# Performance work log

Measured on AMD Instinct MI355X. Metric: run time of the kernel, lower is better.

The kernel has to match this reference:

```python
import jax, jax.numpy as jnp
import numpy as np

ALPHA = 1.702  # ORT swiglu activation constant


def setup_inputs() -> dict:
    key = jax.random.key(0)
    ks = jax.random.split(key, 6)
    B, S, H, I, E = 4, 1024, 2048, 2048, 8
    return {
        "hidden_states": jax.random.normal(ks[0], (B, S, H), dtype=jnp.float32),
        "gate_w": jax.random.normal(ks[1], (E, H), dtype=jnp.float32) * 0.02,
        "fc1_w": jax.random.normal(ks[2], (E, 2 * I, H), dtype=jnp.float32) * 0.02,
        "fc1_b": jax.random.normal(ks[3], (E, 2 * I), dtype=jnp.float32) * 0.02,
        "fc2_w": jax.random.normal(ks[4], (E, H, I), dtype=jnp.float32) * 0.02,
        "fc2_b": jax.random.normal(ks[5], (E, H), dtype=jnp.float32) * 0.02,
        "top_k": 2,
    }


def reference(hidden_states, gate_w, fc1_w, fc1_b, fc2_w, fc2_b, top_k):
    B, S, H = hidden_states.shape
    E = gate_w.shape[0]
    x = hidden_states.reshape(-1, H)                      # [T, H]
    T = x.shape[0]

    # Router: softmax -> top-k -> renormalize selected weights
    logits = jnp.einsum("th,eh->te", x, gate_w)           # [T, E]
    probs = jax.nn.softmax(logits, axis=-1)
    top_vals, top_idx = jax.lax.top_k(probs, top_k)       # [T, k]
    top_vals = top_vals / jnp.sum(top_vals, axis=-1, keepdims=True)
    # Dense combine weights [T, E] (zero for non-selected experts)
    combine = jnp.zeros((T, E), dtype=x.dtype).at[
        jnp.arange(T)[:, None], top_idx
    ].add(top_vals)

    # Expert FC1 (packed gate/linear, interleaved) -> swiglu -> FC2
    h = jnp.einsum("th,efh->etf", x, fc1_w) + fc1_b[:, None, :]   # [E, T, 2I]
    g = h[..., 0::2]                                              # gate part [E, T, I]
    l = h[..., 1::2]                                              # linear part [E, T, I]
    a = g * jax.nn.sigmoid(ALPHA * g) * (l + 1.0)                 # [E, T, I]
    y = jnp.einsum("eti,ehi->eth", a, fc2_w) + fc2_b[:, None, :]  # [E, T, H]

    out = jnp.einsum("te,eth->th", combine, y)            # weighted combine
    return out.reshape(B, S, H)
```

## Files before the change

### kernel.cpp

```cpp
#include <hip/hip_runtime.h>
#include <math.h>


#define T_TOK 4096
#define H_DIM 2048
#define I_DIM 2048
#define F_DIM 4096
#define E_NUM 8
#define ALPHA_C 1.702f
#define ALPHA_LOG2E 2.4554674f

#define TILE_M 64
#define KT 32
#define ACT_CAP_F (2 * T_TOK + E_NUM * TILE_M)
#define BTM 128
#define ACT_CAP_B (2 * T_TOK + E_NUM * BTM)

#define GATE_BLOCKS (T_TOK / 4)
#define CVT_BLOCKS  16384

typedef unsigned short ushort_t;
typedef __attribute__((ext_vector_type(8))) unsigned short ushort8v;
typedef __attribute__((ext_vector_type(8))) __bf16 bf16x8;
typedef __attribute__((ext_vector_type(4))) float f32x4;

__device__ __forceinline__ ushort_t f2bf(float f) {
    unsigned int u = __float_as_uint(f);
    unsigned int r = (u + 0x7FFFu + ((u >> 16) & 1u)) >> 16;
    return (ushort_t)r;
}
__device__ __forceinline__ float bf2f(ushort_t b) {
    return __uint_as_float(((unsigned int)b) << 16);
}

__device__ __forceinline__ void gl_lds16(const ushort_t* g, ushort_t* l) {
    __builtin_amdgcn_global_load_lds(
        (const __attribute__((address_space(1))) void*)g,
        (__attribute__((address_space(3))) void*)l, 16, 0, 0);
}

__global__ __launch_bounds__(256) void prep_kernel(
    const float* __restrict__ x, const float* __restrict__ gw,
    const float* __restrict__ w1, const float* __restrict__ w2,
    ushort_t* __restrict__ wb, ushort_t* __restrict__ xb,
    int* __restrict__ tok, int4* __restrict__ tidx, float2* __restrict__ twgt,
    int* __restrict__ cnt, int n1g, int ntg) {
    if (blockIdx.x < GATE_BLOCKS) {
        int t = blockIdx.x * 4 + (threadIdx.x >> 6);
        int lane = threadIdx.x & 63;
        const float* xr = x + (size_t)t * H_DIM;
        ushort_t* xbr = xb + (size_t)t * H_DIM;
        float acc[E_NUM];
#pragma unroll
        for (int e = 0; e < E_NUM; e++) acc[e] = 0.f;
#pragma unroll
        for (int i = 0; i < H_DIM / 256; i++) {
            int j = (i * 64 + lane) * 4;
            float4 xv = *(const float4*)(xr + j);
            *(ushort4*)(xbr + j) =
                make_ushort4(f2bf(xv.x), f2bf(xv.y), f2bf(xv.z), f2bf(xv.w));
#pragma unroll
            for (int e = 0; e < E_NUM; e++) {
                float4 g = *(const float4*)(gw + e * H_DIM + j);
                acc[e] += xv.x * g.x + xv.y * g.y + xv.z * g.z + xv.w * g.w;
            }
        }
#pragma unroll
        for (int e = 0; e < E_NUM; e++) {
#pragma unroll
            for (int s = 32; s > 0; s >>= 1) acc[e] += __shfl_xor(acc[e], s, 64);
        }
        if (lane == 0) {
            int i0 = 0; float b0 = acc[0];
            for (int e = 1; e < E_NUM; e++) if (acc[e] > b0) { b0 = acc[e]; i0 = e; }
            int i1 = -1; float b1 = -3.0e38f;
            for (int e = 0; e < E_NUM; e++) {
                if (e == i0) continue;
                if (acc[e] > b1) { b1 = acc[e]; i1 = e; }
            }
            float e10 = expf(b1 - b0);
            float w0 = 1.f / (1.f + e10);
            float w1v = 1.f - w0;
            int p0 = atomicAdd(&cnt[i0], 1);
            tok[i0 * T_TOK + p0] = t;
            int p1 = atomicAdd(&cnt[i1], 1);
            tok[i1 * T_TOK + p1] = t;
            tidx[t] = make_int4(i0, p0, i1, p1);
            twgt[t] = make_float2(w0, w1v);
        }
    } else {
        int idx = (blockIdx.x - GATE_BLOCKS) * 256 + threadIdx.x;
        int stride = CVT_BLOCKS * 256;
        for (int i = idx; i < ntg; i += stride) {
            const float* s = (i < n1g) ? (w1 + (size_t)i * 8)
                                       : (w2 + ((size_t)(i - n1g)) * 8);
            float4 v0 = *(const float4*)s;
            float4 v1 = *(const float4*)(s + 4);
            ushort8v o;
            o[0] = f2bf(v0.x); o[1] = f2bf(v0.y); o[2] = f2bf(v0.z); o[3] = f2bf(v0.w);
            o[4] = f2bf(v1.x); o[5] = f2bf(v1.y); o[6] = f2bf(v1.z); o[7] = f2bf(v1.w);
            *(ushort8v*)(wb + (size_t)i * 8) = o;
        }
    }
}

__device__ __forceinline__ void calc_off(const int* __restrict__ cnt, int e,
                                         int& off_e, int& cpad_e) {
    int o = 0, cp = 0;
#pragma unroll
    for (int q = 0; q < E_NUM; q++) {
        int c = (cnt[q] + BTM - 1) & ~(BTM - 1);
        if (q < e) o += c;
        if (q == e) cp = c;
    }
    off_e = o; cpad_e = cp;
}

__global__ __launch_bounds__(256, 3) void fc1_mfma(
    const ushort_t* __restrict__ xb, const ushort_t* __restrict__ w1b,
    const float* __restrict__ b1, const int* __restrict__ tok,
    const int* __restrict__ cnt, ushort_t* __restrict__ act) {
    int e = blockIdx.y >> 5;
    int tile = blockIdx.y & 31;
    int off_e, cpad_e;
    calc_off(cnt, e, off_e, cpad_e);
    if (tile * BTM >= cpad_e) return;
    int i0 = blockIdx.x * 64;

    __shared__ ushort_t As[2][128 * 32];
    __shared__ ushort_t Bg[2][64 * 32];
    __shared__ ushort_t Bl[2][64 * 32];

    int tid = threadIdx.x;
    int lane = tid & 63;
    int ww = tid >> 6;
    int wm = ww & 1, wn = ww >> 1;
    int l15 = lane & 15, quad = lane >> 4;
    int r4 = lane >> 2;
    int koff = (lane & 3) * 8;

    const int* tlist = tok + e * T_TOK + tile * BTM;
    int ar0 = ww * 32 + r4;
    const ushort_t* a0 = xb + (size_t)tlist[ar0] * H_DIM + koff;
    const ushort_t* a1 = xb + (size_t)tlist[ar0 + 16] * H_DIM + koff;
    int il = ww * 16 + r4;
    const ushort_t* bsrc = w1b + ((size_t)e * F_DIM + 2 * (i0 + il)) * H_DIM + koff;

    ushort_t* ad0a = &As[0][(ww * 32) * 32];
    ushort_t* ad0b = &As[0][(ww * 32 + 16) * 32];
    ushort_t* ad1a = &As[1][(ww * 32) * 32];
    ushort_t* ad1b = &As[1][(ww * 32 + 16) * 32];
    ushort_t* bg0 = &Bg[0][(ww * 16) * 32];
    ushort_t* bg1 = &Bg[1][(ww * 16) * 32];
    ushort_t* bl0 = &Bl[0][(ww * 16) * 32];
    ushort_t* bl1 = &Bl[1][(ww * 16) * 32];

    f32x4 zf = {0.f, 0.f, 0.f, 0.f};
    f32x4 accg[4][2], accl[4][2];
#pragma unroll
    for (int mc = 0; mc < 4; mc++)
#pragma unroll
        for (int nc = 0; nc < 2; nc++) { accg[mc][nc] = zf; accl[mc][nc] = zf; }

    for (int k0 = 0; k0 < H_DIM; k0 += 64) {
        __syncthreads();
        gl_lds16(a0, ad0a);
        gl_lds16(a1, ad0b);
        gl_lds16(a0 + 32, ad1a);
        gl_lds16(a1 + 32, ad1b);
        gl_lds16(bsrc, bg0);
        gl_lds16(bsrc + 32, bg1);
        gl_lds16(bsrc + H_DIM, bl0);
        gl_lds16(bsrc + H_DIM + 32, bl1);
        a0 += 64; a1 += 64; bsrc += 64;
        __syncthreads();

#pragma unroll
        for (int kk = 0; kk < 2; kk++) {
            bf16x8 af[4], bgf[2], blf[2];
#pragma unroll
            for (int mc = 0; mc < 4; mc++)
                af[mc] = *(const bf16x8*)&As[kk][(wm * 64 + mc * 16 + l15) * 32 + quad * 8];
#pragma unroll
            for (int nc = 0; nc < 2; nc++) {
                bgf[nc] = *(const bf16x8*)&Bg[kk][(wn * 32 + nc * 16 + l15) * 32 + quad * 8];
                blf[nc] = *(const bf16x8*)&Bl[kk][(wn * 32 + nc * 16 + l15) * 32 + quad * 8];
            }
#pragma unroll
            for (int mc = 0; mc < 4; mc++)
#pragma unroll
                for (int nc = 0; nc < 2; nc++) {
                    accg[mc][nc] = __builtin_amdgcn_mfma_f32_16x16x32_bf16(
                        af[mc], bgf[nc], accg[mc][nc], 0, 0, 0);
                    accl[mc][nc] = __builtin_amdgcn_mfma_f32_16x16x32_bf16(
                        af[mc], blf[nc], accl[mc][nc], 0, 0, 0);
                }
        }
    }

    int rowbase = off_e + tile * BTM + wm * 64;
    int colbase = i0 + wn * 32;
    float bgc[2], blc[2];
#pragma unroll
    for (int nc = 0; nc < 2; nc++) {
        int i = colbase + nc * 16 + l15;
        bgc[nc] = b1[(size_t)e * F_DIM + 2 * i];
        blc[nc] = b1[(size_t)e * F_DIM + 2 * i + 1];
    }
#pragma unroll
    for (int mc = 0; mc < 4; mc++)
#pragma unroll
        for (int nc = 0; nc < 2; nc++) {
            int i = colbase + nc * 16 + l15;
#pragma unroll
            for (int r = 0; r < 4; r++) {
                int m = rowbase + mc * 16 + quad * 4 + r;
                float g = accg[mc][nc][r] + bgc[nc];
                float l = accl[mc][nc][r] + blc[nc];
                float s = __builtin_amdgcn_rcpf(
                    1.f + __builtin_amdgcn_exp2f(-ALPHA_LOG2E * g));
                act[(size_t)m * I_DIM + i] = f2bf(g * s * (l + 1.f));
            }
        }
}

__global__ __launch_bounds__(256, 3) void fc2_mfma(
    const ushort_t* __restrict__ act, const ushort_t* __restrict__ w2b,
    const float* __restrict__ b2, const int* __restrict__ cnt,
    ushort_t* __restrict__ ybuf) {
    int e = blockIdx.y >> 5;
    int tile = blockIdx.y & 31;
    int off_e, cpad_e;
    calc_off(cnt, e, off_e, cpad_e);
    if (tile * BTM >= cpad_e) return;
    int h0 = blockIdx.x * 128;
    int rowbase = off_e + tile * BTM;

    __shared__ ushort_t As[2][128 * 32];
    __shared__ ushort_t Bs[2][128 * 32];

    int tid = threadIdx.x;
    int lane = tid & 63;
    int ww = tid >> 6;
    int wm = ww & 1, wn = ww >> 1;
    int l15 = lane & 15, quad = lane >> 4;
    int r4 = lane >> 2;
    int koff = (lane & 3) * 8;

    int ar = ww * 32 + r4;
    const ushort_t* a0 = act + (size_t)(rowbase + ar) * I_DIM + koff;
    const ushort_t* a1 = a0 + (size_t)16 * I_DIM;
    const ushort_t* b0 = w2b + ((size_t)e * H_DIM + h0 + ar) * I_DIM + koff;
    const ushort_t* b1p = b0 + (size_t)16 * I_DIM;

    ushort_t* ad0a = &As[0][(ww * 32) * 32];
    ushort_t* ad0b = &As[0][(ww * 32 + 16) * 32];
    ushort_t* ad1a = &As[1][(ww * 32) * 32];
    ushort_t* ad1b = &As[1][(ww * 32 + 16) * 32];
    ushort_t* bd0a = &Bs[0][(ww * 32) * 32];
    ushort_t* bd0b = &Bs[0][(ww * 32 + 16) * 32];
    ushort_t* bd1a = &Bs[1][(ww * 32) * 32];
    ushort_t* bd1b = &Bs[1][(ww * 32 + 16) * 32];

    f32x4 zf = {0.f, 0.f, 0.f, 0.f};
    f32x4 acc[4][4];
#pragma unroll
    for (int mc = 0; mc < 4; mc++)
#pragma unroll
        for (int nc = 0; nc < 4; nc++) acc[mc][nc] = zf;

    for (int k0 = 0; k0 < I_DIM; k0 += 64) {
        __syncthreads();
        gl_lds16(a0, ad0a);
        gl_lds16(a1, ad0b);
        gl_lds16(a0 + 32, ad1a);
        gl_lds16(a1 + 32, ad1b);
        gl_lds16(b0, bd0a);
        gl_lds16(b1p, bd0b);
        gl_lds16(b0 + 32, bd1a);
        gl_lds16(b1p + 32, bd1b);
        a0 += 64; a1 += 64; b0 += 64; b1p += 64;
        __syncthreads();

#pragma unroll
        for (int kk = 0; kk < 2; kk++) {
            bf16x8 af[4], bf[4];
#pragma unroll
            for (int mc = 0; mc < 4; mc++)
                af[mc] = *(const bf16x8*)&As[kk][(wm * 64 + mc * 16 + l15) * 32 + quad * 8];
#pragma unroll
            for (int nc = 0; nc < 4; nc++)
                bf[nc] = *(const bf16x8*)&Bs[kk][(wn * 64 + nc * 16 + l15) * 32 + quad * 8];
#pragma unroll
            for (int mc = 0; mc < 4; mc++)
#pragma unroll
                for (int nc = 0; nc < 4; nc++)
                    acc[mc][nc] = __builtin_amdgcn_mfma_f32_16x16x32_bf16(
                        af[mc], bf[nc], acc[mc][nc], 0, 0, 0);
        }
    }

    float bc[4];
#pragma unroll
    for (int nc = 0; nc < 4; nc++)
        bc[nc] = b2[(size_t)e * H_DIM + h0 + wn * 64 + nc * 16 + l15];
#pragma unroll
    for (int mc = 0; mc < 4; mc++)
#pragma unroll
        for (int nc = 0; nc < 4; nc++) {
            int h = h0 + wn * 64 + nc * 16 + l15;
#pragma unroll
            for (int r = 0; r < 4; r++) {
                int m = rowbase + wm * 64 + mc * 16 + quad * 4 + r;
                ybuf[(size_t)m * H_DIM + h] = f2bf(acc[mc][nc][r] + bc[nc]);
            }
        }
}

__global__ __launch_bounds__(256) void combine_kernel(
    const ushort_t* __restrict__ ybuf, const int4* __restrict__ tidx,
    const float2* __restrict__ twgt, const int* __restrict__ cnt,
    float* __restrict__ out) {
    int t = blockIdx.x;
    int4 idx = tidx[t];
    float2 w = twgt[t];
    int offv[E_NUM];
    {
        int o = 0;
#pragma unroll
        for (int q = 0; q < E_NUM; q++) {
            offv[q] = o;
            o += (cnt[q] + BTM - 1) & ~(BTM - 1);
        }
    }
    size_t r0 = (size_t)offv[idx.x] + idx.y;
    size_t r1 = (size_t)offv[idx.z] + idx.w;
    int h = threadIdx.x * 8;
    ushort8v a = *(const ushort8v*)(ybuf + r0 * H_DIM + h);
    ushort8v b = *(const ushort8v*)(ybuf + r1 * H_DIM + h);
    float* op = out + (size_t)t * H_DIM + h;
#pragma unroll
    for (int q = 0; q < 8; q++)
        op[q] = w.x * bf2f(a[q]) + w.y * bf2f(b[q]);
}

__global__ __launch_bounds__(64) void gate_fb(
    const float* __restrict__ x, const float* __restrict__ gw,
    int* __restrict__ tok, float* __restrict__ wgt,
    int4* __restrict__ tidx, float2* __restrict__ twgt, int* __restrict__ cnt) {
    int t = blockIdx.x;
    int lane = threadIdx.x;
    const float* xr = x + (size_t)t * H_DIM;
    float acc[E_NUM];
#pragma unroll
    for (int e = 0; e < E_NUM; e++) acc[e] = 0.f;
    for (int j = lane; j < H_DIM; j += 64) {
        float xv = xr[j];
#pragma unroll
        for (int e = 0; e < E_NUM; e++) acc[e] += xv * gw[e * H_DIM + j];
    }
#pragma unroll
    for (int e = 0; e < E_NUM; e++) {
#pragma unroll
        for (int s = 32; s > 0; s >>= 1) acc[e] += __shfl_xor(acc[e], s, 64);
    }
    if (lane == 0) {
        int i0 = 0; float b0 = acc[0];
        for (int e = 1; e < E_NUM; e++) if (acc[e] > b0) { b0 = acc[e]; i0 = e; }
        int i1 = -1; float b1 = -3.0e38f;
        for (int e = 0; e < E_NUM; e++) {
            if (e == i0) continue;
            if (acc[e] > b1) { b1 = acc[e]; i1 = e; }
        }
        float e10 = expf(b1 - b0);
        float w0 = 1.f / (1.f + e10);
        float w1 = 1.f - w0;
        int p0 = atomicAdd(&cnt[i0], 1);
        tok[i0 * T_TOK + p0] = t; wgt[i0 * T_TOK + p0] = w0;
        int p1 = atomicAdd(&cnt[i1], 1);
        tok[i1 * T_TOK + p1] = t; wgt[i1 * T_TOK + p1] = w1;
        tidx[t] = make_int4(i0, p0, i1, p1);
        twgt[t] = make_float2(w0, w1);
    }
}

__global__ __launch_bounds__(256) void pad_kernel(
    int* __restrict__ tok, float* __restrict__ wgt,
    const int* __restrict__ cnt, int* __restrict__ cnt_pad,
    int* __restrict__ off, int tile) {
    __shared__ int s_cnt[E_NUM], s_pad[E_NUM];
    if (threadIdx.x == 0) {
        int o = 0;
        for (int e = 0; e < E_NUM; e++) {
            int c = cnt[e];
            int cp = (c + tile - 1) / tile * tile;
            s_cnt[e] = c; s_pad[e] = cp;
            cnt_pad[e] = cp;
            off[e] = o;
            o += cp;
        }
    }
    __syncthreads();
    for (int e = 0; e < E_NUM; e++) {
        for (int p = s_cnt[e] + (int)threadIdx.x; p < s_pad[e]; p += 256) {
            tok[e * T_TOK + p] = 0;
            wgt[e * T_TOK + p] = 0.f;
        }
    }
}

__global__ __launch_bounds__(256) void fc1_kernel(
    const float* __restrict__ x, const float* __restrict__ w1,
    const float* __restrict__ b1, const int* __restrict__ tok,
    const int* __restrict__ cnt_pad, const int* __restrict__ off,
    ushort_t* __restrict__ act) {
    int e = blockIdx.y >> 6;
    int tile = blockIdx.y & 63;
    if (tile * TILE_M >= cnt_pad[e]) return;
    int i0 = blockIdx.x * 64;
    int f0 = i0 * 2;

    __shared__ float xs[KT][TILE_M + 4];
    __shared__ float wsh[KT][128 + 4];

    int tid = threadIdx.x;
    int tx = tid & 15, ty = tid >> 4;
    int rloc = tid >> 3;
    int c4 = (tid & 7) * 4;

    const int* tlist = tok + e * T_TOK + tile * TILE_M;
    int tk0 = tlist[rloc];
    int tk1 = tlist[rloc + 32];
    const float* xp0 = x + (size_t)tk0 * H_DIM + c4;
    const float* xp1 = x + (size_t)tk1 * H_DIM + c4;
    const float* wp = w1 + ((size_t)e * F_DIM + f0 + rloc) * H_DIM + c4;

    float ga[4][4] = {{0.f}}, la[4][4] = {{0.f}};

    for (int k0 = 0; k0 < H_DIM; k0 += KT) {
        __syncthreads();
        {
            float4 v0 = *(const float4*)(xp0 + k0);
            float4 v1 = *(const float4*)(xp1 + k0);
            xs[c4 + 0][rloc] = v0.x; xs[c4 + 1][rloc] = v0.y;
            xs[c4 + 2][rloc] = v0.z; xs[c4 + 3][rloc] = v0.w;
            xs[c4 + 0][rloc + 32] = v1.x; xs[c4 + 1][rloc + 32] = v1.y;
            xs[c4 + 2][rloc + 32] = v1.z; xs[c4 + 3][rloc + 32] = v1.w;
        }
        {
#pragma unroll
            for (int r = 0; r < 4; r++) {
                float4 v = *(const float4*)(wp + (size_t)(32 * r) * H_DIM + k0);
                int fr = rloc + 32 * r;
                wsh[c4 + 0][fr] = v.x; wsh[c4 + 1][fr] = v.y;
                wsh[c4 + 2][fr] = v.z; wsh[c4 + 3][fr] = v.w;
            }
        }
        __syncthreads();
#pragma unroll
        for (int k = 0; k < KT; k++) {
            float4 xv = *(const float4*)&xs[k][ty * 4];
            float4 wa = *(const float4*)&wsh[k][tx * 8];
            float4 wb = *(const float4*)&wsh[k][tx * 8 + 4];
            float xm[4] = {xv.x, xv.y, xv.z, xv.w};
            float gg[4] = {wa.x, wa.z, wb.x, wb.z};
            float ll[4] = {wa.y, wa.w, wb.y, wb.w};
#pragma unroll
            for (int m = 0; m < 4; m++)
#pragma unroll
                for (int n = 0; n < 4; n++) {
                    ga[m][n] += xm[m] * gg[n];
                    la[m][n] += xm[m] * ll[n];
                }
        }
    }

    int rowbase = off[e] + tile * TILE_M;
    float bg[4], bl[4];
#pragma unroll
    for (int n = 0; n < 4; n++) {
        int i = i0 + tx * 4 + n;
        bg[n] = b1[(size_t)e * F_DIM + 2 * i];
        bl[n] = b1[(size_t)e * F_DIM + 2 * i + 1];
    }
#pragma unroll
    for (int m = 0; m < 4; m++) {
        int row = rowbase + ty * 4 + m;
        ushort_t us[4];
#pragma unroll
        for (int n = 0; n < 4; n++) {
            float g = ga[m][n] + bg[n];
            float l = la[m][n] + bl[n];
            float s = 1.f / (1.f + expf(-ALPHA_C * g));
            us[n] = f2bf(g * s * (l + 1.f));
        }
        *(ushort4*)&act[(size_t)row * I_DIM + i0 + tx * 4] =
            make_ushort4(us[0], us[1], us[2], us[3]);
    }
}

__global__ __launch_bounds__(256) void fc2_kernel(
    const ushort_t* __restrict__ act, const float* __restrict__ w2,
    const float* __restrict__ b2, const int* __restrict__ tok,
    const float* __restrict__ wgt, const int* __restrict__ cnt_pad,
    const int* __restrict__ off, float* __restrict__ out) {
    int e = blockIdx.y >> 6;
    int tile = blockIdx.y & 63;
    if (tile * TILE_M >= cnt_pad[e]) return;
    int h0 = blockIdx.x * 64;

    __shared__ float as_[KT][TILE_M + 4];
    __shared__ float wsh[KT][64 + 4];

    int tid = threadIdx.x;
    int tx = tid & 15, ty = tid >> 4;
    int rowbase = off[e] + tile * TILE_M;

    int arow = tid >> 2;
    int ac8 = (tid & 3) * 8;
    const ushort_t* ap = act + (size_t)(rowbase + arow) * I_DIM + ac8;
    int rloc = tid >> 3;
    int c4 = (tid & 7) * 4;
    const float* wp = w2 + ((size_t)e * H_DIM + h0 + rloc) * I_DIM + c4;

    float acc[4][4] = {{0.f}};

    for (int k0 = 0; k0 < I_DIM; k0 += KT) {
        __syncthreads();
        {
            ushort8v v = *(const ushort8v*)(ap + k0);
#pragma unroll
            for (int q = 0; q < 8; q++) as_[ac8 + q][arow] = bf2f(v[q]);
        }
        {
#pragma unroll
            for (int r = 0; r < 2; r++) {
                float4 v = *(const float4*)(wp + (size_t)(32 * r) * I_DIM + k0);
                int hr = rloc + 32 * r;
                wsh[c4 + 0][hr] = v.x; wsh[c4 + 1][hr] = v.y;
                wsh[c4 + 2][hr] = v.z; wsh[c4 + 3][hr] = v.w;
            }
        }
        __syncthreads();
#pragma unroll
        for (int k = 0; k < KT; k++) {
            float4 xv = *(const float4*)&as_[k][ty * 4];
            float4 wv = *(const float4*)&wsh[k][tx * 4];
            float xm[4] = {xv.x, xv.y, xv.z, xv.w};
            float wn[4] = {wv.x, wv.y, wv.z, wv.w};
#pragma unroll
            for (int m = 0; m < 4; m++)
#pragma unroll
                for (int n = 0; n < 4; n++) acc[m][n] += xm[m] * wn[n];
        }
    }

    const int* tlist = tok + e * T_TOK + tile * TILE_M;
    const float* wlist = wgt + e * T_TOK + tile * TILE_M;
#pragma unroll
    for (int m = 0; m < 4; m++) {
        int row = ty * 4 + m;
        int t = tlist[row];
        float w = wlist[row];
        if (w == 0.f) continue;
#pragma unroll
        for (int n = 0; n < 4; n++) {
            int h = h0 + tx * 4 + n;
            float y = acc[m][n] + b2[(size_t)e * H_DIM + h];
            atomicAdd(out + (size_t)t * H_DIM + h, w * y);
        }
    }
}

extern "C" void kernel_launch(void* const* d_in, const int* in_sizes, int n_in,
                              void* d_out, int out_size, void* d_ws, size_t ws_size,
                              hipStream_t stream) {
    const float* x  = (const float*)d_in[0];
    const float* gw = (const float*)d_in[1];
    const float* w1 = (const float*)d_in[2];
    const float* b1 = (const float*)d_in[3];
    const float* w2 = (const float*)d_in[4];
    const float* b2 = (const float*)d_in[5];
    float* out = (float*)d_out;
    char* ws = (char*)d_ws;

    size_t w1b_sz = (size_t)E_NUM * F_DIM * H_DIM * 2;
    size_t w2b_sz = (size_t)E_NUM * H_DIM * I_DIM * 2;
    size_t xb_sz  = (size_t)T_TOK * H_DIM * 2;
    size_t act_sz = (size_t)ACT_CAP_B * I_DIM * 2;
    size_t tok_sz = (size_t)E_NUM * T_TOK * 4;
    size_t tidx_sz = (size_t)T_TOK * 16;
    size_t twgt_sz = (size_t)T_TOK * 8;
    size_t need_big = w1b_sz + w2b_sz + xb_sz + act_sz + tok_sz + 64 +
                      tidx_sz + twgt_sz + 256;

    if (ws_size >= need_big) {
        ushort_t* w1b = (ushort_t*)ws;
        ushort_t* w2b = (ushort_t*)(ws + w1b_sz);
        ushort_t* xb  = (ushort_t*)(ws + w1b_sz + w2b_sz);
        ushort_t* act = (ushort_t*)(ws + w1b_sz + w2b_sz + xb_sz);
        char* p = ws + w1b_sz + w2b_sz + xb_sz + act_sz;
        int*    tok  = (int*)p;                 p += tok_sz;
        int*    cnt  = (int*)p;                 p += 64;
        int4*   tidx = (int4*)p;                p += tidx_sz;
        float2* twgt = (float2*)p;
        ushort_t* ybuf = w1b;

        int n1g = (int)(w1b_sz / 16);
        int ntg = n1g + (int)(w2b_sz / 16);

        hipMemsetAsync(tok, 0, tok_sz + 64, stream);
        prep_kernel<<<GATE_BLOCKS + CVT_BLOCKS, 256, 0, stream>>>(
            x, gw, w1, w2, w1b, xb, tok, tidx, twgt, cnt, n1g, ntg);
        fc1_mfma<<<dim3(I_DIM / 64, E_NUM * 32), 256, 0, stream>>>(
            xb, w1b, b1, tok, cnt, act);
        fc2_mfma<<<dim3(H_DIM / 128, E_NUM * 32), 256, 0, stream>>>(
            act, w2b, b2, cnt, ybuf);
        combine_kernel<<<T_TOK, 256, 0, stream>>>(ybuf, tidx, twgt, cnt, out);
        return;
    }

    size_t actB = (size_t)ACT_CAP_F * I_DIM * 2;
    ushort_t* act = (ushort_t*)ws;
    char* p = ws + actB;
    int*    tok  = (int*)p;     p += tok_sz;
    float*  wgt  = (float*)p;   p += tok_sz;
    int4*   tidx = (int4*)p;    p += tidx_sz;
    float2* twgt = (float2*)p;  p += twgt_sz;
    int*    cnt  = (int*)p;
    int*    cnt_pad = cnt + E_NUM;
    int*    off  = cnt_pad + E_NUM;
    size_t need = actB + 2 * tok_sz + tidx_sz + twgt_sz + 256;
    if (ws_size < need) return;

    hipMemsetAsync(cnt, 0, E_NUM * sizeof(int), stream);
    hipMemsetAsync(d_out, 0, (size_t)T_TOK * H_DIM * sizeof(float), stream);
    gate_fb<<<T_TOK, 64, 0, stream>>>(x, gw, tok, wgt, tidx, twgt, cnt);
    pad_kernel<<<1, 256, 0, stream>>>(tok, wgt, cnt, cnt_pad, off, TILE_M);
    fc1_kernel<<<dim3(I_DIM / 64, E_NUM * 64), 256, 0, stream>>>(
        x, w1, b1, tok, cnt_pad, off, act);
    fc2_kernel<<<dim3(H_DIM / 64, E_NUM * 64), 256, 0, stream>>>(
        act, w2, b2, tok, wgt, cnt_pad, off, out);
}
```

Before: 840.5 us.

## Move FC2 weight conversion into FC1 kernel and widen conversion per thread

The fp32-to-bf16 conversion of the FC2 weights moves out of the prep kernel and into extra blocks appended to the FC1 grid, so it overlaps with FC1 matrix work instead of lengthening prep. The remaining FC1 weight conversion now handles 32 elements per thread using nontemporal loads, with fewer conversion blocks. The aim is to hide the memory-bound conversion behind compute. In exchange the extra blocks compete with FC1 tiles for bandwidth and compute units, and the 3-blocks-per-CU launch bound still applies to the conversion blocks.

```diff
diff --git a/kernel.cpp b/kernel.cpp
--- a/kernel.cpp
+++ b/kernel.cpp
@@ -17,7 +17,10 @@
 #define ACT_CAP_B (2 * T_TOK + E_NUM * BTM)
 
 #define GATE_BLOCKS (T_TOK / 4)
-#define CVT_BLOCKS  16384
+#define CVT_BLOCKS  4096
+#define N1Q 2097152
+#define N2Q 1048576
+#define W2X 8
 
 typedef unsigned short ushort_t;
 typedef __attribute__((ext_vector_type(8))) unsigned short ushort8v;
@@ -39,12 +42,27 @@
         (__attribute__((address_space(3))) void*)l, 16, 0, 0);
 }
 
+__device__ __forceinline__ void cvt32(const float* __restrict__ s,
+                                      ushort_t* __restrict__ d) {
+    f32x4 v[8];
+#pragma unroll
+    for (int j = 0; j < 8; j++)
+        v[j] = __builtin_nontemporal_load((const f32x4*)(s + 4 * j));
+#pragma unroll
+    for (int g = 0; g < 4; g++) {
+        ushort8v o;
+#pragma unroll
+        for (int k = 0; k < 8; k++)
+            o[k] = f2bf(v[2 * g + (k >> 2)][k & 3]);
+        *(ushort8v*)(d + 8 * g) = o;
+    }
+}
+
 __global__ __launch_bounds__(256) void prep_kernel(
     const float* __restrict__ x, const float* __restrict__ gw,
-    const float* __restrict__ w1, const float* __restrict__ w2,
-    ushort_t* __restrict__ wb, ushort_t* __restrict__ xb,
-    int* __restrict__ tok, int4* __restrict__ tidx, float2* __restrict__ twgt,
-    int* __restrict__ cnt, int n1g, int ntg) {
+    const float* __restrict__ w1, ushort_t* __restrict__ wb,
+    ushort_t* __restrict__ xb, int* __restrict__ tok, int4* __restrict__ tidx,
+    float2* __restrict__ twgt, int* __restrict__ cnt) {
     if (blockIdx.x < GATE_BLOCKS) {
         int t = blockIdx.x * 4 + (threadIdx.x >> 6);
         int lane = threadIdx.x & 63;
@@ -89,18 +107,10 @@
             twgt[t] = make_float2(w0, w1v);
         }
     } else {
-        int idx = (blockIdx.x - GATE_BLOCKS) * 256 + threadIdx.x;
-        int stride = CVT_BLOCKS * 256;
-        for (int i = idx; i < ntg; i += stride) {
-            const float* s = (i < n1g) ? (w1 + (size_t)i * 8)
-                                       : (w2 + ((size_t)(i - n1g)) * 8);
-            float4 v0 = *(const float4*)s;
-            float4 v1 = *(const float4*)(s + 4);
-            ushort8v o;
-            o[0] = f2bf(v0.x); o[1] = f2bf(v0.y); o[2] = f2bf(v0.z); o[3] = f2bf(v0.w);
-            o[4] = f2bf(v1.x); o[5] = f2bf(v1.y); o[6] = f2bf(v1.z); o[7] = f2bf(v1.w);
-            *(ushort8v*)(wb + (size_t)i * 8) = o;
-        }
+        int idx = (int)(blockIdx.x - GATE_BLOCKS) * 256 + (int)threadIdx.x;
+        const int stride = CVT_BLOCKS * 256;
+        for (int q = idx; q < N1Q; q += stride)
+            cvt32(w1 + (size_t)q * 32, wb + (size_t)q * 32);
     }
 }
 
@@ -119,7 +129,16 @@
 __global__ __launch_bounds__(256, 3) void fc1_mfma(
     const ushort_t* __restrict__ xb, const ushort_t* __restrict__ w1b,
     const float* __restrict__ b1, const int* __restrict__ tok,
-    const int* __restrict__ cnt, ushort_t* __restrict__ act) {
+    const int* __restrict__ cnt, ushort_t* __restrict__ act,
+    const float* __restrict__ w2f, ushort_t* __restrict__ w2b) {
+    if (blockIdx.x >= I_DIM / 64) {
+        int flat = (int)(blockIdx.x - I_DIM / 64) * 256 + (int)blockIdx.y;
+        int idx = flat * 256 + (int)threadIdx.x;
+        const int stride = W2X * 256 * 256;
+        for (int q = idx; q < N2Q; q += stride)
+            cvt32(w2f + (size_t)q * 32, w2b + (size_t)q * 32);
+        return;
+    }
     int e = blockIdx.y >> 5;
     int tile = blockIdx.y & 31;
     int off_e, cpad_e;
@@ -606,14 +625,11 @@
         float2* twgt = (float2*)p;
         ushort_t* ybuf = w1b;
 
-        int n1g = (int)(w1b_sz / 16);
-        int ntg = n1g + (int)(w2b_sz / 16);
-
         hipMemsetAsync(tok, 0, tok_sz + 64, stream);
         prep_kernel<<<GATE_BLOCKS + CVT_BLOCKS, 256, 0, stream>>>(
-            x, gw, w1, w2, w1b, xb, tok, tidx, twgt, cnt, n1g, ntg);
-        fc1_mfma<<<dim3(I_DIM / 64, E_NUM * 32), 256, 0, stream>>>(
-            xb, w1b, b1, tok, cnt, act);
+            x, gw, w1, w1b, xb, tok, tidx, twgt, cnt);
+        fc1_mfma<<<dim3(I_DIM / 64 + W2X, E_NUM * 32), 256, 0, stream>>>(
+            xb, w1b, b1, tok, cnt, act, w2, w2b);
         fc2_mfma<<<dim3(H_DIM / 128, E_NUM * 32), 256, 0, stream>>>(
             act, w2b, b2, cnt, ybuf);
         combine_kernel<<<T_TOK, 256, 0, stream>>>(ybuf, tidx, twgt, cnt, out);
```

Measured after the change: 943.5 us. 12.3% more time.
